# Performance work log

Measured on AMD Instinct MI355X. Metric: run time of the kernel, lower is better.

## Reference

```python
import jax, jax.numpy as jnp
import numpy as np

N = 100000
E = 1600000
IN_DIM = 128
OUT_DIM = 64


def setup_inputs() -> dict:
    key = jax.random.key(0)
    k_h, k_ei, k_ew, k_W, k_a = jax.random.split(key, 5)
    h = jax.random.normal(k_h, (N, IN_DIM), dtype=jnp.float32)
    edge_index = jax.random.randint(k_ei, (2, E), 0, N, dtype=jnp.int64)
    edge_weight = jax.random.uniform(k_ew, (E,), dtype=jnp.float32)
    # nn.Linear weights (Kaiming-uniform-ish scale)
    W = jax.random.uniform(k_W, (OUT_DIM, IN_DIM), dtype=jnp.float32,
                           minval=-1.0, maxval=1.0) / np.sqrt(IN_DIM)
    a = jax.random.uniform(k_a, (2 * OUT_DIM,), dtype=jnp.float32,
                           minval=-1.0, maxval=1.0) / np.sqrt(2 * OUT_DIM)
    return {"h": h, "edge_index": edge_index, "edge_weight": edge_weight,
            "W": W, "a": a}


def reference(h, edge_index, edge_weight, W, a):
    # Faithful translation of _GATConvSparse.forward (inference; dropout = identity).
    n = h.shape[0]
    src, dst = edge_index[0], edge_index[1]
    Wh = h @ W.T                                  # (N, out_dim)
    d = Wh.shape[1]
    # a(cat([Wh[src], Wh[dst]])) == Wh[src] @ a[:d] + Wh[dst] @ a[d:]
    alpha = Wh[src] @ a[:d] + Wh[dst] @ a[d:]     # (E,)
    alpha = alpha * edge_weight
    # Buggy-but-faithful 'softmax': segment-sum raw scores onto dst nodes...
    alpha_node = jax.ops.segment_sum(alpha, dst, num_segments=n)   # (N,)
    alpha_exp = jnp.exp(alpha_node - alpha_node.max())             # (N,)
    # ...then normalize per-edge exp(src) by sum of exp(src) over each dst segment.
    denom = jax.ops.segment_sum(alpha_exp[src], dst, num_segments=n)  # (N,)
    alpha_norm = alpha_exp[src] / (denom[dst] + 1e-9)              # (E,)
    out = jax.ops.segment_sum(alpha_norm[:, None] * Wh[src], dst,
                              num_segments=n)                      # (N, out_dim)
    return jax.nn.elu(out)
```

## Files before the change

### kernel.cpp

```cpp
#include <hip/hip_runtime.h>
#include <math.h>

#define Nn 100000
#define Ee 1600000
#define IND 128
#define OUTD 64
#define DPB 64
#define NB 1563
#define BSTR 1280
#define CAP 1536
#define GB 1563
#define ECHUNK 2048
#define EB_BLOCKS 782
#define CSCAN_BLOCKS 196
#define AFIX 1048576.0f

using bf16x8 = __attribute__((ext_vector_type(8))) short;
using f32x4 = __attribute__((ext_vector_type(4))) float;

__device__ __forceinline__ unsigned short f2bf(float f) {
    unsigned u = __float_as_uint(f);
    u = u + 0x7FFFu + ((u >> 16) & 1u);
    return (unsigned short)(u >> 16);
}
__device__ __forceinline__ float bf2f(unsigned short h) {
    return __uint_as_float(((unsigned)h) << 16);
}

__device__ __forceinline__ bool probe64(const void* __restrict__ ei) {
    const long long* p = (const long long*)ei;
    bool ok = true;
#pragma unroll
    for (int i = 0; i < 8; ++i) {
        long long v = p[i];
        ok = ok && (v >= 0 && v < Nn);
    }
    return ok;
}

__device__ __forceinline__ void load_edge(const void* ei, int e, bool is64,
                                          int& s, int& d) {
    if (is64) {
        const long long* p = (const long long*)ei;
        s = (int)p[e];
        d = (int)p[Ee + e];
    } else {
        const int* p = (const int*)ei;
        s = p[e];
        d = p[Ee + e];
    }
}

__device__ __forceinline__ int load_dst(const void* ei, int e, bool is64) {
    if (is64) return (int)((const long long*)ei)[Ee + e];
    return ((const int*)ei)[Ee + e];
}

__global__ __launch_bounds__(512) void k_hist(
    const void* __restrict__ ei, unsigned short* __restrict__ counts) {
    __shared__ int cnt[NB];
    int t = threadIdx.x;
    int hc = blockIdx.x;
    for (int i = t; i < NB; i += 512) cnt[i] = 0;
    __syncthreads();
    bool is64 = probe64(ei);
    int base = hc * ECHUNK;
#pragma unroll
    for (int i = 0; i < 4; ++i) {
        int e = base + i * 512 + t;
        if (e < Ee) atomicAdd(&cnt[load_dst(ei, e, is64) >> 6], 1);
    }
    __syncthreads();
    for (int i = t; i < NB; i += 512)
        counts[(size_t)hc * NB + i] = (unsigned short)cnt[i];
}

__global__ __launch_bounds__(512) void k_cscan(
    unsigned short* __restrict__ counts, int* __restrict__ bcnt) {
    int gw = (int)((blockIdx.x * 512 + threadIdx.x) >> 6);
    int lane = threadIdx.x & 63;
    if (gw >= NB) return;
    int run = 0;
    for (int c0 = 0; c0 < EB_BLOCKS; c0 += 64) {
        int c = c0 + lane;
        int v = (c < EB_BLOCKS) ? (int)counts[(size_t)c * NB + gw] : 0;
        int s = v;
#pragma unroll
        for (int d = 1; d < 64; d <<= 1) {
            int u = __shfl_up(s, d, 64);
            if (lane >= d) s += u;
        }
        if (c < EB_BLOCKS)
            counts[(size_t)c * NB + gw] = (unsigned short)(run + s - v);
        run += __shfl(s, 63, 64);
    }
    if (lane == 0) bcnt[gw] = run;
}

__global__ __launch_bounds__(256) void k_gemm(
    const float* __restrict__ h, const float* __restrict__ W,
    const float* __restrict__ a, unsigned short* __restrict__ Whb,
    float* __restrict__ s1, float* __restrict__ s2) {
    __shared__ unsigned short Ash[64][136];
    __shared__ unsigned short Wsh[64][136];
    __shared__ float al[2 * OUTD];
    int bid = blockIdx.x;
    int t = threadIdx.x;

    int R = bid * 64;
    for (int i = t; i < 2048; i += 256) {
        float4 v = ((const float4*)W)[i];
        int r = i >> 5, c = (i & 31) << 2;
        unsigned lo = (unsigned)f2bf(v.x) | ((unsigned)f2bf(v.y) << 16);
        unsigned hi = (unsigned)f2bf(v.z) | ((unsigned)f2bf(v.w) << 16);
        *(uint2*)&Wsh[r][c] = make_uint2(lo, hi);
    }
    if (t < 32) ((float4*)al)[t] = ((const float4*)a)[t];
    for (int i = t; i < 2048; i += 256) {
        int r = i >> 5, c = (i & 31) << 2;
        int n = R + r;
        float4 v = make_float4(0.f, 0.f, 0.f, 0.f);
        if (n < Nn) v = ((const float4*)(h + (size_t)n * IND))[i & 31];
        unsigned lo = (unsigned)f2bf(v.x) | ((unsigned)f2bf(v.y) << 16);
        unsigned hi = (unsigned)f2bf(v.z) | ((unsigned)f2bf(v.w) << 16);
        *(uint2*)&Ash[r][c] = make_uint2(lo, hi);
    }
    __syncthreads();

    int w = t >> 6, l = t & 63;
    int li = l & 15, lg = l >> 4;
    f32x4 acc[4];
#pragma unroll
    for (int nt = 0; nt < 4; ++nt) acc[nt] = (f32x4){0.f, 0.f, 0.f, 0.f};
#pragma unroll
    for (int kk = 0; kk < 4; ++kk) {
        bf16x8 af = *(const bf16x8*)&Ash[w * 16 + li][kk * 32 + lg * 8];
#pragma unroll
        for (int nt = 0; nt < 4; ++nt) {
            bf16x8 bf = *(const bf16x8*)&Wsh[nt * 16 + li][kk * 32 + lg * 8];
            acc[nt] = __builtin_amdgcn_mfma_f32_16x16x32_bf16(af, bf,
                                                              acc[nt],
                                                              0, 0, 0);
        }
    }
    float p1[4] = {0.f, 0.f, 0.f, 0.f};
    float p2[4] = {0.f, 0.f, 0.f, 0.f};
#pragma unroll
    for (int nt = 0; nt < 4; ++nt) {
        float a1v = al[nt * 16 + li];
        float a2v = al[OUTD + nt * 16 + li];
#pragma unroll
        for (int r = 0; r < 4; ++r) {
            float v = acc[nt][r];
            p1[r] += v * a1v;
            p2[r] += v * a2v;
            int row = R + w * 16 + lg * 4 + r;
            if (row < Nn)
                Whb[(size_t)row * OUTD + nt * 16 + li] = f2bf(v);
        }
    }
#pragma unroll
    for (int r = 0; r < 4; ++r) {
#pragma unroll
        for (int m = 1; m < 16; m <<= 1) {
            p1[r] += __shfl_xor(p1[r], m, 64);
            p2[r] += __shfl_xor(p2[r], m, 64);
        }
    }
    if (li < 4) {
        int row = R + w * 16 + lg * 4 + li;
        if (row < Nn) {
            s1[row] = p1[li];
            s2[row] = p2[li];
        }
    }
}

__global__ __launch_bounds__(512) void k_binscatter(
    const void* __restrict__ ei, const float* __restrict__ ew,
    const unsigned short* __restrict__ counts, uint2* __restrict__ bins) {
    __shared__ int cnt[NB];
    __shared__ int gbase[NB];
    int hc = blockIdx.x;
    int t = threadIdx.x;
    for (int i = t; i < NB; i += 512) {
        cnt[i] = 0;
        gbase[i] = (int)counts[(size_t)hc * NB + i];
    }
    __syncthreads();
    bool is64 = probe64(ei);
    int base = hc * ECHUNK;
    unsigned rx[4];
    unsigned rw[4];
    int rb[4];
    int rk[4];
#pragma unroll
    for (int i = 0; i < 4; ++i) {
        int e = base + i * 512 + t;
        rb[i] = -1;
        rx[i] = 0;
        rw[i] = 0;
        rk[i] = 0;
        if (e < Ee) {
            int s, d;
            load_edge(ei, e, is64, s, d);
            rw[i] = __float_as_uint(ew[e]);
            int b = d >> 6;
            rb[i] = b;
            rk[i] = atomicAdd(&cnt[b], 1);
            rx[i] = ((unsigned)s << 7) | ((unsigned)(d & 63) << 24);
        }
    }
    __syncthreads();
#pragma unroll
    for (int i = 0; i < 4; ++i) {
        if (rb[i] >= 0) {
            int off = gbase[rb[i]] + rk[i];
            if (off < BSTR)
                bins[(size_t)rb[i] * BSTR + off] = make_uint2(rx[i], rw[i]);
        }
    }
}

__global__ __launch_bounds__(256) void k_balpha(
    const uint2* __restrict__ bins, const int* __restrict__ bcnt,
    const float* __restrict__ s1, const float* __restrict__ s2,
    float* __restrict__ ae) {
    __shared__ int anl[DPB];
    __shared__ int ews[DPB];
    int b = blockIdx.x;
    int t = threadIdx.x;
    if (t < DPB) {
        anl[t] = 0;
        ews[t] = 0;
    }
    __syncthreads();
    int e0 = b * BSTR;
    int c = bcnt[b];
    int e1 = e0 + (c < BSTR ? c : BSTR);
    for (int k = e0 + t; k < e1; k += 256) {
        uint2 r = bins[k];
        int dloc = (int)(r.x >> 24);
        int s = (int)((r.x >> 7) & 0x1FFFF);
        float w = __uint_as_float(r.y);
        atomicAdd(&anl[dloc], (int)rintf(s1[s] * w * AFIX));
        atomicAdd(&ews[dloc], (int)rintf(w * AFIX));
    }
    __syncthreads();
    if (t < DPB) {
        int n = b * DPB + t;
        if (n < Nn) {
            float an = ((float)anl[t] + s2[n] * (float)ews[t]) * (1.f / AFIX);
            ae[n] = expf(an);
        }
    }
}

#define AGG_BODY(NR)                                                         \
    {                                                                        \
        uint2 rr[NR];                                                        \
        unsigned ww[NR];                                                     \
        _Pragma("unroll") for (int j = 0; j < NR; ++j)                       \
            rr[j] = lp[2 * j];                                               \
        _Pragma("unroll") for (int j = 0; j < NR; ++j)                       \
            ww[j] = *(const unsigned*)(whbB + (rr[j].x + hl4));              \
        _Pragma("unroll") for (int j = 0; j < NR; ++j) {                     \
            float aa = __uint_as_float(rr[j].y);                             \
            acc.x += aa * __uint_as_float(ww[j] << 16);                      \
            acc.y += aa * __uint_as_float(ww[j] & 0xFFFF0000u);              \
            den += aa;                                                       \
        }                                                                    \
        lp += 2 * NR;                                                        \
    }

__global__ __launch_bounds__(512, 4) void k_agg(
    const uint2* __restrict__ bins, const int* __restrict__ bcnt,
    const float* __restrict__ ae, const unsigned short* __restrict__ Whb,
    float* __restrict__ out) {
    __shared__ uint2 lrec[CAP];
    __shared__ int cnt[DPB];
    __shared__ int sbase[DPB];
    int b = blockIdx.x;
    int t = threadIdx.x;
    int lane = t & 63;
    int wave = t >> 6;
    int half = lane >> 5;
    int hl = lane & 31;
    unsigned hl4 = (unsigned)hl << 2;
    int e0 = b * BSTR;
    int c = bcnt[b];
    int total = c < BSTR ? c : BSTR;
    int e1 = e0 + total;
    const char* whbB = (const char*)Whb;

    if (t < DPB) cnt[t] = 0;
    __syncthreads();

    unsigned su[CAP / 512];
    float sa[CAP / 512];
    int srk[CAP / 512];
#pragma unroll
    for (int i = 0; i < CAP / 512; ++i) {
        int k = e0 + i * 512 + t;
        srk[i] = -1;
        if (k < e1) {
            uint2 r = bins[k];
            srk[i] = atomicAdd(&cnt[r.x >> 24], 1);
            su[i] = r.x;
            sa[i] = ae[(r.x >> 7) & 0x1FFFF];
        }
    }
    __syncthreads();
    if (t < DPB) {
        int v = cnt[t];
#pragma unroll
        for (int d = 1; d < DPB; d <<= 1) {
            int u = __shfl_up(v, d, 64);
            if (t >= d) v += u;
        }
        sbase[t] = v;
    }
    __syncthreads();
#pragma unroll
    for (int i = 0; i < CAP / 512; ++i) {
        if (srk[i] >= 0) {
            int dloc = su[i] >> 24;
            int pos = sbase[dloc] - cnt[dloc] + srk[i];
            lrec[pos] = make_uint2(su[i] & 0x00FFFF80u,
                                   __float_as_uint(sa[i]));
        }
    }
    __syncthreads();

    for (int d = wave * 8; d < wave * 8 + 8; ++d) {
        int k1 = sbase[d];
        int k = k1 - cnt[d];
        const uint2* lp = lrec + k + half;
        float2 acc = make_float2(0.f, 0.f);
        float den = 0.f;
        for (; k + 15 < k1; k += 16) AGG_BODY(8);
        for (; k + 7 < k1; k += 8) AGG_BODY(4);
        for (; k + 1 < k1; k += 2) AGG_BODY(1);
        if (k < k1) {
            uint2 rA = lrec[k];
            unsigned wA = *(const unsigned*)(whbB + (rA.x + hl4));
            float aA = half ? 0.f : __uint_as_float(rA.y);
            acc.x += aA * __uint_as_float(wA << 16);
            acc.y += aA * __uint_as_float(wA & 0xFFFF0000u);
            den += aA;
        }
        float ax = acc.x + __shfl_xor(acc.x, 32, 64);
        float ay = acc.y + __shfl_xor(acc.y, 32, 64);
        float dn = den + __shfl_xor(den, 32, 64);
        if (half == 0) {
            int n = b * DPB + d;
            if (n < Nn) {
                float inv = 1.f / (dn + 1e-9f);
                float vx = ax * inv;
                float vy = ay * inv;
                vx = vx > 0.f ? vx : expm1f(vx);
                vy = vy > 0.f ? vy : expm1f(vy);
                *(float2*)&out[(size_t)n * OUTD + hl * 2] =
                    make_float2(vx, vy);
            }
        }
    }
}

extern "C" void kernel_launch(void* const* d_in, const int* in_sizes, int n_in,
                              void* d_out, int out_size, void* d_ws,
                              size_t ws_size, hipStream_t stream) {
    const float* h = (const float*)d_in[0];
    const void* ei = d_in[1];
    const float* ew = (const float*)d_in[2];
    const float* W = (const float*)d_in[3];
    const float* a = (const float*)d_in[4];
    float* out = (float*)d_out;

    unsigned short* Whb = (unsigned short*)d_ws;
    float* s1 = (float*)(Whb + (size_t)Nn * OUTD);
    float* s2 = s1 + Nn;
    float* ae = s2 + Nn;
    int* bcnt = (int*)(ae + Nn);
    uint2* bins = (uint2*)(bcnt + 2048);
    unsigned short* counts =
        (unsigned short*)(bins + (size_t)NB * BSTR);

    k_hist<<<EB_BLOCKS, 512, 0, stream>>>(ei, counts);
    k_cscan<<<CSCAN_BLOCKS, 512, 0, stream>>>(counts, bcnt);
    k_gemm<<<GB, 256, 0, stream>>>(h, W, a, Whb, s1, s2);
    k_binscatter<<<EB_BLOCKS, 512, 0, stream>>>(ei, ew, counts, bins);
    k_balpha<<<NB, 256, 0, stream>>>(bins, bcnt, s1, s2, ae);
    k_agg<<<NB, 512, 0, stream>>>(bins, bcnt, ae, Whb, out);
}
```

Before: 121.7 us.

## Stage binscatter records in LDS sorted by bin for coalesced global writes

```diff
diff --git a/kernel.cpp b/kernel.cpp
--- a/kernel.cpp
+++ b/kernel.cpp
@@ -10,8 +10,8 @@
 #define BSTR 1280
 #define CAP 1536
 #define GB 1563
-#define ECHUNK 2048
-#define EB_BLOCKS 782
+#define ECHUNK 4096
+#define EB_BLOCKS 391
 #define CSCAN_BLOCKS 196
 #define AFIX 1048576.0f
 
@@ -56,22 +56,22 @@
     return ((const int*)ei)[Ee + e];
 }
 
-__global__ __launch_bounds__(512) void k_hist(
+__global__ __launch_bounds__(256) void k_hist(
     const void* __restrict__ ei, unsigned short* __restrict__ counts) {
     __shared__ int cnt[NB];
     int t = threadIdx.x;
     int hc = blockIdx.x;
-    for (int i = t; i < NB; i += 512) cnt[i] = 0;
+    for (int i = t; i < NB; i += 256) cnt[i] = 0;
     __syncthreads();
     bool is64 = probe64(ei);
     int base = hc * ECHUNK;
 #pragma unroll
-    for (int i = 0; i < 4; ++i) {
-        int e = base + i * 512 + t;
+    for (int i = 0; i < 16; ++i) {
+        int e = base + i * 256 + t;
         if (e < Ee) atomicAdd(&cnt[load_dst(ei, e, is64) >> 6], 1);
     }
     __syncthreads();
-    for (int i = t; i < NB; i += 512)
+    for (int i = t; i < NB; i += 256)
         counts[(size_t)hc * NB + i] = (unsigned short)cnt[i];
 }
 
@@ -181,6 +181,10 @@
     const unsigned short* __restrict__ counts, uint2* __restrict__ bins) {
     __shared__ int cnt[NB];
     __shared__ int gbase[NB];
+    __shared__ int lbase[NB];
+    __shared__ uint2 srec[ECHUNK];
+    __shared__ int saddr[ECHUNK];
+    __shared__ int wsum[9];
     int hc = blockIdx.x;
     int t = threadIdx.x;
     for (int i = t; i < NB; i += 512) {
@@ -190,12 +194,12 @@
     __syncthreads();
     bool is64 = probe64(ei);
     int base = hc * ECHUNK;
-    unsigned rx[4];
-    unsigned rw[4];
-    int rb[4];
-    int rk[4];
-#pragma unroll
-    for (int i = 0; i < 4; ++i) {
+    unsigned rx[8];
+    unsigned rw[8];
+    int rb[8];
+    int rk[8];
+#pragma unroll
+    for (int i = 0; i < 8; ++i) {
         int e = base + i * 512 + t;
         rb[i] = -1;
         rx[i] = 0;
@@ -212,13 +216,53 @@
         }
     }
     __syncthreads();
-#pragma unroll
-    for (int i = 0; i < 4; ++i) {
+    int i0 = t * 4;
+    int c0 = (i0 + 0 < NB) ? cnt[i0 + 0] : 0;
+    int c1 = (i0 + 1 < NB) ? cnt[i0 + 1] : 0;
+    int c2 = (i0 + 2 < NB) ? cnt[i0 + 2] : 0;
+    int c3 = (i0 + 3 < NB) ? cnt[i0 + 3] : 0;
+    int ts = c0 + c1 + c2 + c3;
+    int lane = t & 63;
+    int wv = t >> 6;
+    int ws = ts;
+#pragma unroll
+    for (int d = 1; d < 64; d <<= 1) {
+        int u = __shfl_up(ws, d, 64);
+        if (lane >= d) ws += u;
+    }
+    if (lane == 63) wsum[wv] = ws;
+    __syncthreads();
+    if (t == 0) {
+        int acc = 0;
+#pragma unroll
+        for (int j = 0; j < 8; ++j) {
+            int v = wsum[j];
+            wsum[j] = acc;
+            acc += v;
+        }
+        wsum[8] = acc;
+    }
+    __syncthreads();
+    int tpre = wsum[wv] + (ws - ts);
+    if (i0 + 0 < NB) lbase[i0 + 0] = tpre;
+    if (i0 + 1 < NB) lbase[i0 + 1] = tpre + c0;
+    if (i0 + 2 < NB) lbase[i0 + 2] = tpre + c0 + c1;
+    if (i0 + 3 < NB) lbase[i0 + 3] = tpre + c0 + c1 + c2;
+    int btot = wsum[8];
+    __syncthreads();
+#pragma unroll
+    for (int i = 0; i < 8; ++i) {
         if (rb[i] >= 0) {
+            int slot = lbase[rb[i]] + rk[i];
+            srec[slot] = make_uint2(rx[i], rw[i]);
             int off = gbase[rb[i]] + rk[i];
-            if (off < BSTR)
-                bins[(size_t)rb[i] * BSTR + off] = make_uint2(rx[i], rw[i]);
-        }
+            saddr[slot] = (off < BSTR) ? (rb[i] * BSTR + off) : -1;
+        }
+    }
+    __syncthreads();
+    for (int i = t; i < btot; i += 512) {
+        int a = saddr[i];
+        if (a >= 0) bins[a] = srec[i];
     }
 }
 
@@ -386,7 +430,7 @@
     unsigned short* counts =
         (unsigned short*)(bins + (size_t)NB * BSTR);
 
-    k_hist<<<EB_BLOCKS, 512, 0, stream>>>(ei, counts);
+    k_hist<<<EB_BLOCKS, 256, 0, stream>>>(ei, counts);
     k_cscan<<<CSCAN_BLOCKS, 512, 0, stream>>>(counts, bcnt);
     k_gemm<<<GB, 256, 0, stream>>>(h, W, a, Whb, s1, s2);
     k_binscatter<<<EB_BLOCKS, 512, 0, stream>>>(ei, ew, counts, bins);
```

Result: faster. 110.1 us (-9.5%).
